# Performance work log

Hardware: AMD Instinct MI355X
Metric: run time of the kernel (lower is better)

Reference implementation:

```python
import jax, jax.numpy as jnp
import numpy as np

B = 8
NF = 64
COUNTS = [1200, 1400, 1500, 1536, 1600, 1700, 1800, 1552]  # ragged per-batch point counts
ND = 12288  # total decoder points (= sum(COUNTS))
NE = 12288  # total encoder points
LQ = 1800   # max per-batch count (padding length)
EPS = 1e-4  # scn BatchNormalization eps


def _build_geometry():
    """Random sparse 3D voxel coords per batch on a 64^3 grid; parent cells (coord//2)
    are unique by construction so the stride-2 downsample keeps one point per cell
    and Nkv == Nd with the same per-batch ordering (matches the module's slicing)."""
    rng = np.random.default_rng(0)
    coords = []
    for b, c in enumerate(COUNTS):
        cells = rng.choice(32 * 32 * 32, size=c, replace=False)
        x, y, z = cells // 1024, (cells // 32) % 32, cells % 32
        off = rng.integers(0, 2, size=(c, 3))
        pts = np.stack([x, y, z], 1) * 2 + off
        coords.append(np.concatenate([np.full((c, 1), b), pts], 1))
    coords = np.concatenate(coords, 0)  # [ND, 4] = (batch, x, y, z)
    lut = {tuple(r): i for i, r in enumerate(coords)}
    offs = np.array([[dx, dy, dz] for dx in (-1, 0, 1) for dy in (-1, 0, 1) for dz in (-1, 0, 1)])
    nbr = np.full((ND, 27), -1, np.int32)  # 3^3 submanifold rulebook
    for i, r in enumerate(coords):
        for k, o in enumerate(offs):
            j = lut.get((r[0], r[1] + o[0], r[2] + o[1], r[3] + o[2]))
            if j is not None:
                nbr[i, k] = j
    kv_nbr = np.full((ND, 8), -1, np.int32)  # stride-2 2^3 conv rulebook (1 child per cell)
    off_id = (coords[:, 1] % 2) * 4 + (coords[:, 2] % 2) * 2 + (coords[:, 3] % 2)
    kv_nbr[np.arange(ND), off_id] = np.arange(ND)
    pad_idx = np.full((B, LQ), -1, np.int32)
    unpad_idx = np.zeros(ND, np.int32)
    s = 0
    for b, c in enumerate(COUNTS):
        pad_idx[b, :c] = np.arange(s, s + c)
        unpad_idx[s:s + c] = b * LQ + np.arange(c)
        s += c
    return nbr, kv_nbr, pad_idx, unpad_idx


def setup_inputs() -> dict:
    nbr, kv_nbr, pad_idx, unpad_idx = _build_geometry()
    key = jax.random.key(0)
    ks = jax.random.split(key, 16)
    w = lambda k, i, o: jax.random.normal(k, (i, o), jnp.float32) / np.sqrt(i)
    w3 = lambda k, t, i, o: jax.random.normal(k, (t, i, o), jnp.float32) / np.sqrt(t * i)
    return {
        "x_decoder": jax.random.normal(ks[0], (ND, NF), jnp.float32),
        "x_encoder": jax.random.normal(ks[1], (NE, NF), jnp.float32),
        "Wp1": w(ks[2], NF, NF), "Wq": w(ks[3], NF, NF), "Wk": w(ks[4], NF, NF),
        "Wv": w(ks[5], NF, NF), "Wt": w(ks[6], NF, NF), "Wq1": w(ks[7], NF, NF),
        "Wk1": w(ks[8], NF, NF), "Wv1": w(ks[9], NF, NF),
        "Wdown": w3(ks[10], 8, NF, NF),
        "W3t": w3(ks[11], 27, NF, NF), "W3a": w3(ks[12], 27, NF, NF), "W3b": w3(ks[13], 27, NF, NF),
        "bn_gamma": jnp.ones((6, NF), jnp.float32),
        "bn_beta": jnp.zeros((6, NF), jnp.float32),
        "nbr": jnp.asarray(nbr), "kv_nbr": jnp.asarray(kv_nbr),
        "pad_idx": jnp.asarray(pad_idx), "unpad_idx": jnp.asarray(unpad_idx),
    }


def _bn(x, g, b):  # training-mode scn.BatchNormalization over all active points
    m = jnp.mean(x, 0)
    v = jnp.mean(jnp.square(x - m), 0)
    return (x - m) * jax.lax.rsqrt(v + EPS) * g + b


def _gconv(f, idx, W):  # rulebook sparse conv: idx [N,K] (-1 = missing), W [K,F,O]
    mask = (idx >= 0).astype(f.dtype)[..., None]
    g = f[jnp.clip(idx, 0)] * mask  # [N, K, F]
    return jnp.einsum('nkf,kfo->no', g, W)


def _pad(f, pad_idx):  # flat [N,F] -> padded [B,L,F] + validity mask [B,L]
    m = pad_idx >= 0
    return f[jnp.clip(pad_idx, 0)] * m[..., None].astype(f.dtype), m


def reference(x_decoder, x_encoder, Wp1, Wq, Wk, Wv, Wt, Wq1, Wk1, Wv1,
              Wdown, W3t, W3a, W3b, bn_gamma, bn_beta,
              nbr, kv_nbr, pad_idx, unpad_idx):
    xd = x_decoder @ Wp1                      # p1 (1x1 submanifold conv)
    q = xd @ Wq
    ke = x_encoder @ Wk
    ve = x_encoder @ Wv
    # Stage-1 cross attention. The torch loop slices queries per batch but always
    # uses the FULL encoder K/V (dk = features.T), so it equals one global attention.
    attn = jax.nn.softmax(q @ ke.T, axis=-1)  # [ND, NE], no 1/sqrt(d) scaling in source
    xr = (attn @ ve) @ Wt                     # trans_conv (1x1)
    xd = xd + _bn(xr, bn_gamma[0], bn_beta[0])  # after_norm residual add

    q1 = xd @ Wq1
    kv = _bn(_gconv(q1, kv_nbr, Wdown), bn_gamma[1], bn_beta[1])  # stride-2 conv + BN
    k1 = kv @ Wk1
    v1 = kv @ Wv1
    # Stage-2 ragged per-batch self attention (Nkv == Nd by construction).
    qp, _ = _pad(q1, pad_idx)                 # [B, LQ, NF]
    kp, mkv = _pad(k1, pad_idx)
    vp, _ = _pad(v1, pad_idx)
    s2 = jnp.einsum('blf,bmf->blm', qp, kp)
    s2 = jnp.where(mkv[:, None, :], s2, jnp.float32(-1e30))
    o = jnp.einsum('blm,bmf->blf', jax.nn.softmax(s2, axis=-1), vp)
    xr2 = o.reshape(B * LQ, NF)[unpad_idx]    # back to flat ragged layout [ND, NF]
    xr2 = _gconv(xr2, nbr, W3t)               # trans_conv1 (3^3 submanifold conv)
    xd = xd + _bn(xr2, bn_gamma[2], bn_beta[2])  # after_norm1 residual add

    # res block: BNReLU -> conv3 -> BNReLU -> conv3, add identity, BNReLU
    z = _gconv(jax.nn.relu(_bn(xd, bn_gamma[3], bn_beta[3])), nbr, W3a)
    z = _gconv(jax.nn.relu(_bn(z, bn_gamma[4], bn_beta[4])), nbr, W3b)
    return jax.nn.relu(_bn(xd + z, bn_gamma[5], bn_beta[5]))
```

## Files before the change

### kernel.cpp

```cpp
#include <hip/hip_runtime.h>

#define NPTS 12288
#define LQPAD 1800
#define LPAD2 1856
#define EPSBN 1e-4f
#define NSPLIT 8

typedef _Float16 half8 __attribute__((ext_vector_type(8)));
typedef _Float16 half4 __attribute__((ext_vector_type(4)));
typedef float floatx4 __attribute__((ext_vector_type(4)));

__global__ __launch_bounds__(256) void pack_all(const float* Wp1, const float* Wq, const float* Wk,
                                                const float* Wv, const float* Wt_, const float* Wq1,
                                                const float* Wk1, const float* Wv1, const float* Wdown,
                                                const float* W3t, const float* W3a, const float* W3b,
                                                const int* __restrict__ pad_idx, int* __restrict__ counts,
                                                _Float16* __restrict__ Wf) {
    int g = blockIdx.x;
    int t = threadIdx.x;
    if (g >= 97) {
        int b = g - 97;
        int s = 0;
        for (int i = t; i < LQPAD; i += 256) s += (pad_idx[b * LQPAD + i] >= 0) ? 1 : 0;
        for (int off = 32; off > 0; off >>= 1) s += __shfl_xor(s, off);
        if ((t & 63) == 0) atomicAdd(&counts[b], s);
        return;
    }
    int lane = t & 63, fg = t >> 6;
    int quad = lane >> 4, qi = lane & 15;
    if (g == 1) {
        __shared__ float A[4096], Bs[4096];
        for (int i = t; i < 4096; i += 256) {
            A[i] = Wp1[i];
            Bs[i] = Wq[i];
        }
        __syncthreads();
#pragma unroll
        for (int u = 0; u < 2; u++) {
            int frag = fg * 2 + u;
            int s = frag >> 2, ct = frag & 3;
            half8 v;
#pragma unroll
            for (int j = 0; j < 8; j++) {
                int r = s * 32 + quad * 8 + j, c = ct * 16 + qi;
                float acc = 0.f;
#pragma unroll
                for (int k = 0; k < 64; k++) acc += A[r * 64 + k] * Bs[k * 64 + c];
                v[j] = (_Float16)acc;
            }
            *(half8*)(Wf + (size_t)4096 + frag * 512 + lane * 8) = v;
        }
        return;
    }
    const float* src;
    if (g == 0) src = Wp1;
    else if (g == 2) src = Wk;
    else if (g == 3) src = Wv;
    else if (g == 4) src = Wt_;
    else if (g == 5) src = Wq1;
    else if (g == 6) src = Wk1;
    else if (g == 7) src = Wv1;
    else if (g < 16) src = Wdown + (size_t)(g - 8) * 4096;
    else if (g < 43) src = W3t + (size_t)(g - 16) * 4096;
    else if (g < 70) src = W3a + (size_t)(g - 43) * 4096;
    else src = W3b + (size_t)(g - 70) * 4096;
#pragma unroll
    for (int u = 0; u < 2; u++) {
        int frag = fg * 2 + u;
        int s = frag >> 2, ct = frag & 3;
        half8 v;
#pragma unroll
        for (int j = 0; j < 8; j++) v[j] = (_Float16)src[(s * 32 + quad * 8 + j) * 64 + ct * 16 + qi];
        *(half8*)(Wf + (size_t)g * 4096 + frag * 512 + lane * 8) = v;
    }
}

__device__ inline void load_split8(const float* p, half8& hi, half8& lo) {
    float4 a = *(const float4*)p;
    float4 b = *(const float4*)(p + 4);
    float v[8] = {a.x, a.y, a.z, a.w, b.x, b.y, b.z, b.w};
#pragma unroll
    for (int j = 0; j < 8; j++) {
        _Float16 h = (_Float16)v[j];
        hi[j] = h;
        lo[j] = (_Float16)(v[j] - (float)h);
    }
}

__global__ __launch_bounds__(256) void gemm_head(const float* __restrict__ xdec, const float* __restrict__ xenc,
                                                 const _Float16* __restrict__ Wf, float* __restrict__ xd,
                                                 _Float16* __restrict__ Qh,
                                                 _Float16* __restrict__ Kh, _Float16* __restrict__ Vt) {
    int z = blockIdx.y;
    const float* A = (z < 2) ? xdec : xenc;
    const _Float16* Bf = Wf + (size_t)z * 4096;
    int t = threadIdx.x;
    int lane = t & 63, wv = t >> 6;
    int quad = lane >> 4, qi = lane & 15;
    int row0w = blockIdx.x * 64 + wv * 16;
    half8 ah[2], al[2];
#pragma unroll
    for (int s = 0; s < 2; s++) load_split8(A + (size_t)(row0w + qi) * 64 + s * 32 + quad * 8, ah[s], al[s]);
    floatx4 C[4];
#pragma unroll
    for (int ct = 0; ct < 4; ct++) C[ct] = floatx4{0.f, 0.f, 0.f, 0.f};
#pragma unroll
    for (int ct = 0; ct < 4; ct++)
#pragma unroll
        for (int s = 0; s < 2; s++) {
            half8 b = *(const half8*)(Bf + (s * 4 + ct) * 512 + lane * 8);
            C[ct] = __builtin_amdgcn_mfma_f32_16x16x32_f16(ah[s], b, C[ct], 0, 0, 0);
            C[ct] = __builtin_amdgcn_mfma_f32_16x16x32_f16(al[s], b, C[ct], 0, 0, 0);
        }
    int orow = row0w + quad * 4;
    if (z == 0) {
#pragma unroll
        for (int ct = 0; ct < 4; ct++)
#pragma unroll
            for (int r = 0; r < 4; r++) xd[(size_t)(orow + r) * 64 + ct * 16 + qi] = C[ct][r];
    } else if (z == 1) {
#pragma unroll
        for (int ct = 0; ct < 4; ct++)
#pragma unroll
            for (int r = 0; r < 4; r++) Qh[(size_t)(orow + r) * 64 + ct * 16 + qi] = (_Float16)C[ct][r];
    } else if (z == 2) {
#pragma unroll
        for (int ct = 0; ct < 4; ct++)
#pragma unroll
            for (int r = 0; r < 4; r++) Kh[(size_t)(orow + r) * 64 + ct * 16 + qi] = (_Float16)C[ct][r];
    } else {
#pragma unroll
        for (int ct = 0; ct < 4; ct++) {
            half4 o;
#pragma unroll
            for (int r = 0; r < 4; r++) o[r] = (_Float16)C[ct][r];
            *(half4*)(Vt + (size_t)(ct * 16 + qi) * NPTS + orow) = o;
        }
    }
}

__global__ __launch_bounds__(256) void gemm_q1(const float* __restrict__ xr, float* __restrict__ xd,
                                               const _Float16* __restrict__ Bf,
                                               const float* __restrict__ stats,
                                               const float* __restrict__ gamma,
                                               const float* __restrict__ beta,
                                               _Float16* __restrict__ Oh) {
    int t = threadIdx.x;
    int lane = t & 63, wv = t >> 6;
    int quad = lane >> 4, qi = lane & 15;
    int row0w = blockIdx.x * 64 + wv * 16;
    const float inv_n = 1.f / (float)NPTS;
    half8 ah[2], al[2];
#pragma unroll
    for (int s = 0; s < 2; s++) {
        size_t base = (size_t)(row0w + qi) * 64 + s * 32 + quad * 8;
        float4 xa = *(const float4*)(xr + base);
        float4 xb = *(const float4*)(xr + base + 4);
        float4 da = *(const float4*)(xd + base);
        float4 db = *(const float4*)(xd + base + 4);
        float vx[8] = {xa.x, xa.y, xa.z, xa.w, xb.x, xb.y, xb.z, xb.w};
        float vd[8] = {da.x, da.y, da.z, da.w, db.x, db.y, db.z, db.w};
        float vo[8];
#pragma unroll
        for (int j = 0; j < 8; j++) {
            int f = s * 32 + quad * 8 + j;
            float mean = stats[f] * inv_n;
            float var = stats[64 + f] * inv_n - mean * mean;
            float val = vd[j] + (vx[j] - mean) * rsqrtf(var + EPSBN) * gamma[f] + beta[f];
            vo[j] = val;
            _Float16 h = (_Float16)val;
            ah[s][j] = h;
            al[s][j] = (_Float16)(val - (float)h);
        }
        *(float4*)(xd + base) = float4{vo[0], vo[1], vo[2], vo[3]};
        *(float4*)(xd + base + 4) = float4{vo[4], vo[5], vo[6], vo[7]};
    }
    floatx4 C[4];
#pragma unroll
    for (int ct = 0; ct < 4; ct++) C[ct] = floatx4{0.f, 0.f, 0.f, 0.f};
#pragma unroll
    for (int ct = 0; ct < 4; ct++)
#pragma unroll
        for (int s = 0; s < 2; s++) {
            half8 b = *(const half8*)(Bf + (s * 4 + ct) * 512 + lane * 8);
            C[ct] = __builtin_amdgcn_mfma_f32_16x16x32_f16(ah[s], b, C[ct], 0, 0, 0);
            C[ct] = __builtin_amdgcn_mfma_f32_16x16x32_f16(al[s], b, C[ct], 0, 0, 0);
        }
    int orow = row0w + quad * 4;
#pragma unroll
    for (int ct = 0; ct < 4; ct++)
#pragma unroll
        for (int r = 0; r < 4; r++) Oh[(size_t)(orow + r) * 64 + ct * 16 + qi] = (_Float16)C[ct][r];
}

__global__ __launch_bounds__(256) void gemm_kv1(const float* __restrict__ kv, const _Float16* __restrict__ Wfk,
                                                const _Float16* __restrict__ Wfv,
                                                const float* __restrict__ stats, const float* __restrict__ gamma,
                                                const float* __restrict__ beta, const int* __restrict__ unpad,
                                                _Float16* __restrict__ Kh1, _Float16* __restrict__ Vt2) {
    int y = blockIdx.y;
    int t = threadIdx.x;
    int lane = t & 63, wv = t >> 6;
    int quad = lane >> 4, qi = lane & 15;
    int row0w = blockIdx.x * 64 + wv * 16;
    const float inv_n = 1.f / (float)NPTS;
    half8 ah[2], al[2];
#pragma unroll
    for (int s = 0; s < 2; s++) {
        const float* p = kv + (size_t)(row0w + qi) * 64 + s * 32 + quad * 8;
        float4 a = *(const float4*)p;
        float4 b2 = *(const float4*)(p + 4);
        float v[8] = {a.x, a.y, a.z, a.w, b2.x, b2.y, b2.z, b2.w};
#pragma unroll
        for (int j = 0; j < 8; j++) {
            int f = s * 32 + quad * 8 + j;
            float mean = stats[f] * inv_n;
            float var = stats[64 + f] * inv_n - mean * mean;
            float val = (v[j] - mean) * rsqrtf(var + EPSBN) * gamma[f] + beta[f];
            _Float16 h = (_Float16)val;
            ah[s][j] = h;
            al[s][j] = (_Float16)(val - (float)h);
        }
    }
    const _Float16* Bf = y ? Wfv : Wfk;
    floatx4 C[4];
#pragma unroll
    for (int ct = 0; ct < 4; ct++) C[ct] = floatx4{0.f, 0.f, 0.f, 0.f};
#pragma unroll
    for (int ct = 0; ct < 4; ct++)
#pragma unroll
        for (int s = 0; s < 2; s++) {
            half8 b = *(const half8*)(Bf + (s * 4 + ct) * 512 + lane * 8);
            C[ct] = __builtin_amdgcn_mfma_f32_16x16x32_f16(ah[s], b, C[ct], 0, 0, 0);
            C[ct] = __builtin_amdgcn_mfma_f32_16x16x32_f16(al[s], b, C[ct], 0, 0, 0);
        }
    int orow = row0w + quad * 4;
    if (y == 0) {
#pragma unroll
        for (int ct = 0; ct < 4; ct++)
#pragma unroll
            for (int r = 0; r < 4; r++) Kh1[(size_t)(orow + r) * 64 + ct * 16 + qi] = (_Float16)C[ct][r];
    } else {
        int u0 = unpad[orow], u3 = unpad[orow + 3];
        int b0 = u0 / 1800, b3 = u3 / 1800;
        if (u3 == u0 + 3 && b0 == b3) {
            int p0 = u0 - b0 * 1800;
#pragma unroll
            for (int ct = 0; ct < 4; ct++) {
                half4 o;
#pragma unroll
                for (int r = 0; r < 4; r++) o[r] = (_Float16)C[ct][r];
                *(half4*)(Vt2 + ((size_t)b0 * 64 + ct * 16 + qi) * LPAD2 + p0) = o;
            }
        } else {
#pragma unroll
            for (int r = 0; r < 4; r++) {
                int u = unpad[orow + r];
                int b = u / 1800, p = u - b * 1800;
#pragma unroll
                for (int ct = 0; ct < 4; ct++)
                    Vt2[((size_t)b * 64 + ct * 16 + qi) * LPAD2 + p] = (_Float16)C[ct][r];
            }
        }
    }
}

__global__ __launch_bounds__(256) void gconv_mfma(const _Float16* __restrict__ Xh,
                                                  const int* __restrict__ idx,
                                                  const _Float16* __restrict__ Wf,
                                                  float* __restrict__ OUT, int nk,
                                                  const float* Xadd, float* stats_out) {
    __shared__ float s_sum[64], s_ss[64];
    int t = threadIdx.x;
    int lane = t & 63, wv = t >> 6;
    int quad = lane >> 4, qi = lane & 15;
    int bx = blockIdx.x;
    int row0 = (bx >> 1) * 64 + wv * 16;
    int cb = (bx & 1) * 2;
    if (stats_out) {
        if (t < 64) {
            s_sum[t] = 0.f;
            s_ss[t] = 0.f;
        }
        __syncthreads();
    }
    floatx4 Oacc[2];
#pragma unroll
    for (int u = 0; u < 2; u++) Oacc[u] = floatx4{0.f, 0.f, 0.f, 0.f};
    const int* ip = idx + (size_t)(row0 + qi) * nk;
    int j = ip[0];
    half8 a0 = half8{0, 0, 0, 0, 0, 0, 0, 0};
    half8 a1 = half8{0, 0, 0, 0, 0, 0, 0, 0};
    if (j >= 0) {
        a0 = *(const half8*)(Xh + (size_t)j * 64 + quad * 8);
        a1 = *(const half8*)(Xh + (size_t)j * 64 + 32 + quad * 8);
    }
    for (int k = 0; k < nk; k++) {
        half8 n0 = half8{0, 0, 0, 0, 0, 0, 0, 0};
        half8 n1 = half8{0, 0, 0, 0, 0, 0, 0, 0};
        if (k + 1 < nk) {
            int jn = ip[k + 1];
            if (jn >= 0) {
                n0 = *(const half8*)(Xh + (size_t)jn * 64 + quad * 8);
                n1 = *(const half8*)(Xh + (size_t)jn * 64 + 32 + quad * 8);
            }
        }
        const _Float16* wk = Wf + (size_t)k * 4096;
#pragma unroll
        for (int u = 0; u < 2; u++) {
            int ct = cb + u;
            half8 b0 = *(const half8*)(wk + ct * 512 + lane * 8);
            half8 b1 = *(const half8*)(wk + (4 + ct) * 512 + lane * 8);
            Oacc[u] = __builtin_amdgcn_mfma_f32_16x16x32_f16(a0, b0, Oacc[u], 0, 0, 0);
            Oacc[u] = __builtin_amdgcn_mfma_f32_16x16x32_f16(a1, b1, Oacc[u], 0, 0, 0);
        }
        a0 = n0;
        a1 = n1;
    }
    int orow = row0 + quad * 4;
#pragma unroll
    for (int u = 0; u < 2; u++) {
        int ct = cb + u;
#pragma unroll
        for (int r = 0; r < 4; r++) OUT[(size_t)(orow + r) * 64 + ct * 16 + qi] = Oacc[u][r];
    }
    if (stats_out) {
#pragma unroll
        for (int u = 0; u < 2; u++) {
            int f = (cb + u) * 16 + qi;
            float ps = 0.f, pss = 0.f;
#pragma unroll
            for (int r = 0; r < 4; r++) {
                float v = Oacc[u][r];
                if (Xadd) v += Xadd[(size_t)(orow + r) * 64 + f];
                ps += v;
                pss += v * v;
            }
            atomicAdd(&s_sum[f], ps);
            atomicAdd(&s_ss[f], pss);
        }
        __syncthreads();
        if (t < 64) {
            atomicAdd(&stats_out[t], s_sum[t]);
            atomicAdd(&stats_out[64 + t], s_ss[t]);
        }
    }
}

__global__ __launch_bounds__(256) void bn_apply(const float* __restrict__ X, const float* X2,
                                                const float* R, float* OUT, _Float16* OUT16,
                                                const float* __restrict__ stats,
                                                const float* __restrict__ gamma,
                                                const float* __restrict__ beta,
                                                float* stats_out, int n, int do_relu) {
    __shared__ float sh[2][4][64];
    int t = threadIdx.x;
    int f = t & 63, g = t >> 6;
    float inv_n = 1.f / (float)n;
    float mean = stats[f] * inv_n;
    float var = stats[64 + f] * inv_n - mean * mean;
    float rstd = rsqrtf(var + EPSBN);
    float ga = gamma[f], be = beta[f];
    float s = 0.f, ss = 0.f;
    for (int r = blockIdx.x * 4 + g; r < n; r += gridDim.x * 4) {
        size_t i = (size_t)r * 64 + f;
        float v = X[i];
        if (X2) v += X2[i];
        v = (v - mean) * rstd * ga + be;
        if (R) v += R[i];
        if (do_relu) v = fmaxf(v, 0.f);
        if (OUT) OUT[i] = v;
        if (OUT16) OUT16[i] = (_Float16)v;
        s += v;
        ss += v * v;
    }
    if (stats_out) {
        sh[0][g][f] = s;
        sh[1][g][f] = ss;
        __syncthreads();
        if (g == 0) {
            s = sh[0][0][f] + sh[0][1][f] + sh[0][2][f] + sh[0][3][f];
            ss = sh[1][0][f] + sh[1][1][f] + sh[1][2][f] + sh[1][3][f];
            atomicAdd(&stats_out[f], s);
            atomicAdd(&stats_out[64 + f], ss);
        }
    }
}

__global__ __launch_bounds__(256, 3) void flash1_mfma(const _Float16* __restrict__ Qh,
                                                      const _Float16* __restrict__ Kh,
                                                      const _Float16* __restrict__ Vt,
                                                      _Float16* __restrict__ Op,
                                                      float* __restrict__ Ms,
                                                      float* __restrict__ Ls) {
    __shared__ __align__(16) _Float16 KsF[8 * 512];
    __shared__ __align__(16) _Float16 VsF[8 * 512];
    __shared__ __align__(16) _Float16 PTF[4][2 * 1024];
    int t = threadIdx.x;
    int lane = t & 63, wv = t >> 6;
    int quad = lane >> 4, qi = lane & 15;
    int qb = blockIdx.x, sp = blockIdx.y;
    int q0w = qb * 128 + wv * 32;

    half8 qh[2][2];
#pragma unroll
    for (int sub = 0; sub < 2; sub++)
#pragma unroll
        for (int s = 0; s < 2; s++) {
            int qrow = q0w + sub * 16 + qi;
            qh[sub][s] = *(const half8*)(Qh + (size_t)qrow * 64 + s * 32 + quad * 8);
        }
    floatx4 Oacc[2][4];
#pragma unroll
    for (int sub = 0; sub < 2; sub++)
#pragma unroll
        for (int ft = 0; ft < 4; ft++) Oacc[sub][ft] = floatx4{0.f, 0.f, 0.f, 0.f};
    float m_i[2] = {-1e30f, -1e30f}, l_i[2] = {0.f, 0.f};

    for (int it = 0; it < 24; it++) {
        int k0 = sp * 1536 + it * 64;
        __syncthreads();
#pragma unroll
        for (int u = 0; u < 4; u++) {
            int frag = wv + 4 * u;
            if (frag < 8) {
                int kt = frag >> 1, s = frag & 1;
                int key = k0 + kt * 16 + qi;
                *(half8*)(KsF + frag * 512 + lane * 8) =
                    *(const half8*)(Kh + (size_t)key * 64 + s * 32 + quad * 8);
            } else {
                int fr = frag - 8;
                int ft = fr >> 1, s = fr & 1;
                int f = ft * 16 + qi;
                *(half8*)(VsF + fr * 512 + lane * 8) =
                    *(const half8*)(Vt + (size_t)f * NPTS + k0 + s * 32 + quad * 8);
            }
        }
        __syncthreads();
        half8 ka[4][2];
#pragma unroll
        for (int kt = 0; kt < 4; kt++)
#pragma unroll
            for (int s = 0; s < 2; s++) ka[kt][s] = *(const half8*)(KsF + (kt * 2 + s) * 512 + lane * 8);
        floatx4 st[2][4];
#pragma unroll
        for (int sub = 0; sub < 2; sub++)
#pragma unroll
            for (int kt = 0; kt < 4; kt++) {
                floatx4 acc = floatx4{0.f, 0.f, 0.f, 0.f};
#pragma unroll
                for (int s = 0; s < 2; s++)
                    acc = __builtin_amdgcn_mfma_f32_16x16x32_f16(ka[kt][s], qh[sub][s], acc, 0, 0, 0);
                st[sub][kt] = acc;
            }
#pragma unroll
        for (int sub = 0; sub < 2; sub++) {
            float mloc = -1e30f;
#pragma unroll
            for (int kt = 0; kt < 4; kt++)
#pragma unroll
                for (int r = 0; r < 4; r++) mloc = fmaxf(mloc, st[sub][kt][r]);
            mloc = fmaxf(mloc, __shfl_xor(mloc, 16));
            mloc = fmaxf(mloc, __shfl_xor(mloc, 32));
            float m_new = fmaxf(m_i[sub], mloc);
            float ps = 0.f;
#pragma unroll
            for (int kt = 0; kt < 4; kt++) {
                half4 pk;
#pragma unroll
                for (int r = 0; r < 4; r++) {
                    float p = __expf(st[sub][kt][r] - m_new);
                    ps += p;
                    pk[r] = (_Float16)p;
                }
                int s = kt >> 1;
                int qd2 = (kt & 1) * 2 + (quad >> 1);
                *(half4*)(&PTF[wv][sub * 1024 + (s * 64 + qd2 * 16 + qi) * 8 + (quad & 1) * 4]) = pk;
            }
            ps += __shfl_xor(ps, 16);
            ps += __shfl_xor(ps, 32);
            if (m_new > m_i[sub]) {
                float alpha = __expf(m_i[sub] - m_new);
                l_i[sub] = l_i[sub] * alpha + ps;
                m_i[sub] = m_new;
#pragma unroll
                for (int ft = 0; ft < 4; ft++) Oacc[sub][ft] *= alpha;
            } else {
                l_i[sub] += ps;
            }
        }
        half8 pb[2][2];
#pragma unroll
        for (int sub = 0; sub < 2; sub++)
#pragma unroll
            for (int s = 0; s < 2; s++)
                pb[sub][s] = *(const half8*)(&PTF[wv][sub * 1024 + (s * 64 + lane) * 8]);
#pragma unroll
        for (int ft = 0; ft < 4; ft++)
#pragma unroll
            for (int s = 0; s < 2; s++) {
                half8 v = *(const half8*)(VsF + (ft * 2 + s) * 512 + lane * 8);
                Oacc[0][ft] = __builtin_amdgcn_mfma_f32_16x16x32_f16(v, pb[0][s], Oacc[0][ft], 0, 0, 0);
                Oacc[1][ft] = __builtin_amdgcn_mfma_f32_16x16x32_f16(v, pb[1][s], Oacc[1][ft], 0, 0, 0);
            }
    }
#pragma unroll
    for (int sub = 0; sub < 2; sub++) {
#pragma unroll
        for (int ft = 0; ft < 4; ft++) {
            half4 o;
#pragma unroll
            for (int r = 0; r < 4; r++) o[r] = (_Float16)Oacc[sub][ft][r];
            *(half4*)(Op + ((size_t)sp * NPTS + q0w + sub * 16 + qi) * 64 + ft * 16 + quad * 4) = o;
        }
        if (lane < 16) {
            Ms[sp * NPTS + q0w + sub * 16 + lane] = m_i[sub];
            Ls[sp * NPTS + q0w + sub * 16 + lane] = l_i[sub];
        }
    }
}

__global__ __launch_bounds__(256) void merge_gemm(const _Float16* __restrict__ Op,
                                                  const float* __restrict__ Ms, const float* __restrict__ Ls,
                                                  const _Float16* __restrict__ Wtf,
                                                  float* __restrict__ xr, float* __restrict__ stats_out) {
    __shared__ float w12[64][NSPLIT];
    __shared__ float Linv[64];
    __shared__ __align__(16) _Float16 Ah[64 * 72], Al[64 * 72];
    __shared__ float s_sum[64], s_ss[64];
    int t = threadIdx.x;
    int row0 = blockIdx.x * 64;
    if (t < 64) {
        int q = row0 + t;
        float m[NSPLIT], M = -1e30f;
#pragma unroll
        for (int s = 0; s < NSPLIT; s++) {
            m[s] = Ms[s * NPTS + q];
            M = fmaxf(M, m[s]);
        }
        float L = 0.f;
#pragma unroll
        for (int s = 0; s < NSPLIT; s++) {
            float w = __expf(m[s] - M);
            w12[t][s] = w;
            L += Ls[s * NPTS + q] * w;
        }
        Linv[t] = 1.f / L;
        s_sum[t] = 0.f;
        s_ss[t] = 0.f;
    }
    __syncthreads();
    for (int k = 0; k < 4; k++) {
        int i = t + k * 256;
        int qr = i >> 4, f4 = (i & 15) * 4;
        int q = row0 + qr;
        float acc[4] = {0.f, 0.f, 0.f, 0.f};
#pragma unroll
        for (int s = 0; s < NSPLIT; s++) {
            float w = w12[qr][s];
            half4 o = *(const half4*)(Op + ((size_t)s * NPTS + q) * 64 + f4);
#pragma unroll
            for (int c = 0; c < 4; c++) acc[c] += (float)o[c] * w;
        }
        float inv = Linv[qr];
#pragma unroll
        for (int c = 0; c < 4; c++) {
            float val = acc[c] * inv;
            _Float16 h = (_Float16)val;
            Ah[qr * 72 + f4 + c] = h;
            Al[qr * 72 + f4 + c] = (_Float16)(val - (float)h);
        }
    }
    __syncthreads();
    int lane = t & 63, wv = t >> 6;
    int quad = lane >> 4, qi = lane & 15;
    int rloc = wv * 16 + qi;
    half8 ah[2], al[2];
#pragma unroll
    for (int s = 0; s < 2; s++) {
        ah[s] = *(const half8*)(Ah + rloc * 72 + s * 32 + quad * 8);
        al[s] = *(const half8*)(Al + rloc * 72 + s * 32 + quad * 8);
    }
    floatx4 C[4];
#pragma unroll
    for (int ct = 0; ct < 4; ct++) C[ct] = floatx4{0.f, 0.f, 0.f, 0.f};
#pragma unroll
    for (int ct = 0; ct < 4; ct++)
#pragma unroll
        for (int s = 0; s < 2; s++) {
            half8 b = *(const half8*)(Wtf + (s * 4 + ct) * 512 + lane * 8);
            C[ct] = __builtin_amdgcn_mfma_f32_16x16x32_f16(ah[s], b, C[ct], 0, 0, 0);
            C[ct] = __builtin_amdgcn_mfma_f32_16x16x32_f16(al[s], b, C[ct], 0, 0, 0);
        }
    int orow = row0 + wv * 16 + quad * 4;
#pragma unroll
    for (int ct = 0; ct < 4; ct++) {
        int f = ct * 16 + qi;
        float ps = 0.f, pss = 0.f;
#pragma unroll
        for (int r = 0; r < 4; r++) {
            float v = C[ct][r];
            xr[(size_t)(orow + r) * 64 + f] = v;
            ps += v;
            pss += v * v;
        }
        atomicAdd(&s_sum[f], ps);
        atomicAdd(&s_ss[f], pss);
    }
    __syncthreads();
    if (t < 64) {
        atomicAdd(&stats_out[t], s_sum[t]);
        atomicAdd(&stats_out[64 + t], s_ss[t]);
    }
}

__global__ __launch_bounds__(256) void flash2_mfma(const _Float16* __restrict__ Qh,
                                                   const _Float16* __restrict__ Kh,
                                                   const _Float16* __restrict__ Vt2,
                                                   const int* __restrict__ pad_idx,
                                                   const int* __restrict__ counts,
                                                   _Float16* __restrict__ O) {
    int b = blockIdx.y;
    int c = counts[b];
    int qb = blockIdx.x;
    if (qb * 64 >= c) return;
    __shared__ __align__(16) _Float16 KsF[8 * 512];
    __shared__ __align__(16) _Float16 VsF[8 * 512];
    __shared__ __align__(16) _Float16 PTF[4][2 * 512];
    int t = threadIdx.x;
    int lane = t & 63, wv = t >> 6;
    int quad = lane >> 4, qi = lane & 15;
    const int* prow = pad_idx + b * LQPAD;
    int p_q = qb * 64 + wv * 16 + qi;
    int flat_q = (p_q < LQPAD) ? prow[p_q] : -1;

    half8 qh[2];
#pragma unroll
    for (int s = 0; s < 2; s++) {
        qh[s] = (flat_q >= 0) ? *(const half8*)(Qh + (size_t)flat_q * 64 + s * 32 + quad * 8)
                              : half8{0, 0, 0, 0, 0, 0, 0, 0};
    }
    floatx4 Oacc[4];
#pragma unroll
    for (int ft = 0; ft < 4; ft++) Oacc[ft] = floatx4{0.f, 0.f, 0.f, 0.f};
    float m_i = -1e30f, l_i = 0.f;
    const _Float16* VtB = Vt2 + (size_t)b * 64 * LPAD2;

    int nt = (c + 63) >> 6;
    for (int it = 0; it < nt; it++) {
        int k0 = it * 64;
        __syncthreads();
#pragma unroll
        for (int u = 0; u < 4; u++) {
            int frag = wv + 4 * u;
            if (frag < 8) {
                int kt = frag >> 1, s = frag & 1;
                int kp = k0 + kt * 16 + qi;
                int flat = (kp < c) ? prow[kp] : -1;
                int d0 = s * 32 + quad * 8;
                half8 kvv = half8{0, 0, 0, 0, 0, 0, 0, 0};
                if (flat >= 0) kvv = *(const half8*)(Kh + (size_t)flat * 64 + d0);
                *(half8*)(KsF + frag * 512 + lane * 8) = kvv;
            } else {
                int fr = frag - 8;
                int ft = fr >> 1, s = fr & 1;
                int f = ft * 16 + qi;
                int key = k0 + s * 32 + quad * 8;
                *(half8*)(VsF + fr * 512 + lane * 8) = *(const half8*)(VtB + f * LPAD2 + key);
            }
        }
        __syncthreads();
        floatx4 st[4];
#pragma unroll
        for (int kt = 0; kt < 4; kt++) {
            floatx4 acc = floatx4{0.f, 0.f, 0.f, 0.f};
#pragma unroll
            for (int s = 0; s < 2; s++) {
                half8 a = *(const half8*)(KsF + (kt * 2 + s) * 512 + lane * 8);
                acc = __builtin_amdgcn_mfma_f32_16x16x32_f16(a, qh[s], acc, 0, 0, 0);
            }
            st[kt] = acc;
        }
        float mloc = -1e30f;
#pragma unroll
        for (int kt = 0; kt < 4; kt++)
#pragma unroll
            for (int r = 0; r < 4; r++) mloc = fmaxf(mloc, st[kt][r]);
        mloc = fmaxf(mloc, __shfl_xor(mloc, 16));
        mloc = fmaxf(mloc, __shfl_xor(mloc, 32));
        float m_new = fmaxf(m_i, mloc);
        float ps = 0.f;
#pragma unroll
        for (int kt = 0; kt < 4; kt++) {
            half4 pk;
#pragma unroll
            for (int r = 0; r < 4; r++) {
                int kpos = k0 + kt * 16 + quad * 4 + r;
                float p = (kpos < c) ? __expf(st[kt][r] - m_new) : 0.f;
                ps += p;
                pk[r] = (_Float16)p;
            }
            int s = kt >> 1;
            int qd2 = (kt & 1) * 2 + (quad >> 1);
            *(half4*)(&PTF[wv][(s * 64 + qd2 * 16 + qi) * 8 + (quad & 1) * 4]) = pk;
        }
        ps += __shfl_xor(ps, 16);
        ps += __shfl_xor(ps, 32);
        if (m_new > m_i) {
            float alpha = __expf(m_i - m_new);
            l_i = l_i * alpha + ps;
            m_i = m_new;
#pragma unroll
            for (int ft = 0; ft < 4; ft++) Oacc[ft] *= alpha;
        } else {
            l_i += ps;
        }
        half8 pb[2];
#pragma unroll
        for (int s = 0; s < 2; s++) pb[s] = *(const half8*)(&PTF[wv][(s * 64 + lane) * 8]);
#pragma unroll
        for (int ft = 0; ft < 4; ft++)
#pragma unroll
            for (int s = 0; s < 2; s++) {
                half8 a = *(const half8*)(VsF + (ft * 2 + s) * 512 + lane * 8);
                Oacc[ft] = __builtin_amdgcn_mfma_f32_16x16x32_f16(a, pb[s], Oacc[ft], 0, 0, 0);
            }
    }
    if (flat_q >= 0) {
        float inv = 1.f / l_i;
#pragma unroll
        for (int ft = 0; ft < 4; ft++) {
            half4 o;
#pragma unroll
            for (int r = 0; r < 4; r++) o[r] = (_Float16)(Oacc[ft][r] * inv);
            *(half4*)(O + (size_t)flat_q * 64 + ft * 16 + quad * 4) = o;
        }
    }
}

extern "C" void kernel_launch(void* const* d_in, const int* in_sizes, int n_in,
                              void* d_out, int out_size, void* d_ws, size_t ws_size,
                              hipStream_t stream) {
    const float* x_dec = (const float*)d_in[0];
    const float* x_enc = (const float*)d_in[1];
    const float* Wp1 = (const float*)d_in[2];
    const float* Wq = (const float*)d_in[3];
    const float* Wk = (const float*)d_in[4];
    const float* Wv = (const float*)d_in[5];
    const float* Wt_ = (const float*)d_in[6];
    const float* Wq1 = (const float*)d_in[7];
    const float* Wk1 = (const float*)d_in[8];
    const float* Wv1 = (const float*)d_in[9];
    const float* Wdown = (const float*)d_in[10];
    const float* W3t = (const float*)d_in[11];
    const float* W3a = (const float*)d_in[12];
    const float* W3b = (const float*)d_in[13];
    const float* bn_g = (const float*)d_in[14];
    const float* bn_b = (const float*)d_in[15];
    const int* nbr = (const int*)d_in[16];
    const int* kv_nbr = (const int*)d_in[17];
    const int* pad_idx = (const int*)d_in[18];
    const int* unpad_idx = (const int*)d_in[19];
    float* out = (float*)d_out;
    float* ws = (float*)d_ws;

    const int N = NPTS;
    const size_t BUF = (size_t)N * 64;
    float* xd = ws;
    float* s1 = ws + 1 * BUF;
    float* s2 = ws + 2 * BUF;
    float* s3 = ws + 3 * BUF;
    float* s4 = ws + 4 * BUF;
    float* s5 = ws + 5 * BUF;
    float* s6 = ws + 6 * BUF;
    float* s7 = ws + 7 * BUF;
    float* s8 = ws + 8 * BUF;
    float* arena = ws + 9 * BUF;

    float* stats = arena;
    int* counts = (int*)(arena + 768);
    float* Ms = arena + 1024;
    float* Ls = Ms + (size_t)NSPLIT * NPTS;
    _Float16* WfA = (_Float16*)(Ls + (size_t)NSPLIT * NPTS);

    _Float16* Oph = (_Float16*)s1;
    _Float16* Qh = (_Float16*)s7;
    _Float16* Kh = (_Float16*)s8;
    _Float16* Vt = Kh + BUF;
    float* xr = s8;
    _Float16* Qh1 = (_Float16*)s7;
    float* kv = s1;
    _Float16* Kh1 = (_Float16*)s2;
    _Float16* Vt2 = (_Float16*)s3;
    _Float16* z2h = (_Float16*)s4;
    float* xr2 = s5;
    _Float16* xrh = (_Float16*)s6;
    float* o2 = s1;
    _Float16* xr2h = (_Float16*)s2;
    float* z2 = s3;

    const _Float16* Wtf = WfA + 4 * 4096;
    const _Float16* Wq1f = WfA + 5 * 4096;
    const _Float16* Wk1f = WfA + 6 * 4096;
    const _Float16* Wv1f = WfA + 7 * 4096;
    const _Float16* Wdf = WfA + 8 * 4096;
    const _Float16* W3tf = WfA + (size_t)16 * 4096;
    const _Float16* W3af = WfA + (size_t)43 * 4096;
    const _Float16* W3bf = WfA + (size_t)70 * 4096;

    hipMemsetAsync(stats, 0, 1024 * sizeof(float), stream);

    dim3 B(256);
    int gG = N / 64;
    int gC2 = 2 * gG;

    pack_all<<<105, B, 0, stream>>>(Wp1, Wq, Wk, Wv, Wt_, Wq1, Wk1, Wv1, Wdown, W3t, W3a, W3b,
                                    pad_idx, counts, WfA);

    gemm_head<<<dim3(gG, 4), B, 0, stream>>>(x_dec, x_enc, WfA, xd, Qh, Kh, Vt);
    flash1_mfma<<<dim3(N / 128, NSPLIT), B, 0, stream>>>(Qh, Kh, Vt, Oph, Ms, Ls);
    merge_gemm<<<gG, B, 0, stream>>>(Oph, Ms, Ls, Wtf, xr, stats + 0);
    gemm_q1<<<gG, B, 0, stream>>>(xr, xd, Wq1f, stats + 0, bn_g + 0, bn_b + 0, Qh1);

    gconv_mfma<<<gC2, B, 0, stream>>>(Qh1, kv_nbr, Wdf, kv, 8, nullptr, stats + 128);
    gemm_kv1<<<dim3(gG, 2), B, 0, stream>>>(kv, Wk1f, Wv1f, stats + 128, bn_g + 64, bn_b + 64,
                                            unpad_idx, Kh1, Vt2);
    flash2_mfma<<<dim3(LPAD2 / 64, 8), B, 0, stream>>>(Qh1, Kh1, Vt2, pad_idx, counts, z2h);
    gconv_mfma<<<gC2, B, 0, stream>>>(z2h, nbr, W3tf, xr2, 27, nullptr, stats + 256);
    bn_apply<<<256, B, 0, stream>>>(xr2, nullptr, xd, xd, nullptr, stats + 256, bn_g + 128, bn_b + 128,
                                    stats + 384, N, 0);

    bn_apply<<<256, B, 0, stream>>>(xd, nullptr, nullptr, nullptr, xrh, stats + 384, bn_g + 192,
                                    bn_b + 192, nullptr, N, 1);
    gconv_mfma<<<gC2, B, 0, stream>>>(xrh, nbr, W3af, o2, 27, nullptr, stats + 512);
    bn_apply<<<256, B, 0, stream>>>(o2, nullptr, nullptr, nullptr, xr2h, stats + 512, bn_g + 256,
                                    bn_b + 256, nullptr, N, 1);
    gconv_mfma<<<gC2, B, 0, stream>>>(xr2h, nbr, W3bf, z2, 27, xd, stats + 640);
    bn_apply<<<256, B, 0, stream>>>(xd, z2, nullptr, out, nullptr, stats + 640, bn_g + 320, bn_b + 320,
                                    nullptr, N, 1);
}
```

Baseline: 409.3 us.

## Fuse BN+ReLU into gather conv and use exp2 with pre-scaled queries

```diff
diff --git a/kernel.cpp b/kernel.cpp
--- a/kernel.cpp
+++ b/kernel.cpp
@@ -5,6 +5,13 @@
 #define LPAD2 1856
 #define EPSBN 1e-4f
 #define NSPLIT 8
+#define LOG2E 1.44269504088896340736f
+
+#if __has_builtin(__builtin_amdgcn_exp2f)
+#define EXP2F __builtin_amdgcn_exp2f
+#else
+#define EXP2F exp2f
+#endif
 
 typedef _Float16 half8 __attribute__((ext_vector_type(8)));
 typedef _Float16 half4 __attribute__((ext_vector_type(4)));
@@ -122,7 +129,8 @@
 #pragma unroll
         for (int ct = 0; ct < 4; ct++)
 #pragma unroll
-            for (int r = 0; r < 4; r++) Qh[(size_t)(orow + r) * 64 + ct * 16 + qi] = (_Float16)C[ct][r];
+            for (int r = 0; r < 4; r++)
+                Qh[(size_t)(orow + r) * 64 + ct * 16 + qi] = (_Float16)(C[ct][r] * LOG2E);
     } else if (z == 2) {
 #pragma unroll
         for (int ct = 0; ct < 4; ct++)
@@ -344,6 +352,130 @@
             atomicAdd(&stats_out[t], s_sum[t]);
             atomicAdd(&stats_out[64 + t], s_ss[t]);
         }
+    }
+}
+
+__global__ __launch_bounds__(256) void gconv_bn_mfma(const float* __restrict__ X,
+                                                     const int* __restrict__ idx,
+                                                     const _Float16* __restrict__ Wf,
+                                                     float* __restrict__ OUT, int nk,
+                                                     const float* __restrict__ stats,
+                                                     const float* __restrict__ gamma,
+                                                     const float* __restrict__ beta,
+                                                     const float* Xadd, float* stats_out) {
+    __shared__ float s_sum[64], s_ss[64];
+    int t = threadIdx.x;
+    int lane = t & 63, wv = t >> 6;
+    int quad = lane >> 4, qi = lane & 15;
+    int bx = blockIdx.x;
+    int row0 = (bx >> 1) * 64 + wv * 16;
+    int cb = (bx & 1) * 2;
+    if (t < 64) {
+        s_sum[t] = 0.f;
+        s_ss[t] = 0.f;
+    }
+    __syncthreads();
+    const float inv_n = 1.f / (float)NPTS;
+    float sc[2][8], sh[2][8];
+#pragma unroll
+    for (int s = 0; s < 2; s++)
+#pragma unroll
+        for (int jj = 0; jj < 8; jj++) {
+            int f = s * 32 + quad * 8 + jj;
+            float mean = stats[f] * inv_n;
+            float var = stats[64 + f] * inv_n - mean * mean;
+            float rs = rsqrtf(var + EPSBN) * gamma[f];
+            sc[s][jj] = rs;
+            sh[s][jj] = beta[f] - mean * rs;
+        }
+    floatx4 Oacc[2];
+#pragma unroll
+    for (int u = 0; u < 2; u++) Oacc[u] = floatx4{0.f, 0.f, 0.f, 0.f};
+    const int* ip = idx + (size_t)(row0 + qi) * nk;
+    float cur[16];
+    int jvalid;
+    {
+        int j0 = ip[0];
+        jvalid = (j0 >= 0);
+        if (jvalid) {
+            const float* p = X + (size_t)j0 * 64 + quad * 8;
+            float4 x0 = *(const float4*)p;
+            float4 x1 = *(const float4*)(p + 4);
+            float4 x2 = *(const float4*)(p + 32);
+            float4 x3 = *(const float4*)(p + 36);
+            cur[0] = x0.x; cur[1] = x0.y; cur[2] = x0.z; cur[3] = x0.w;
+            cur[4] = x1.x; cur[5] = x1.y; cur[6] = x1.z; cur[7] = x1.w;
+            cur[8] = x2.x; cur[9] = x2.y; cur[10] = x2.z; cur[11] = x2.w;
+            cur[12] = x3.x; cur[13] = x3.y; cur[14] = x3.z; cur[15] = x3.w;
+        }
+    }
+    for (int k = 0; k < nk; k++) {
+        half8 a0, a1;
+        if (jvalid) {
+#pragma unroll
+            for (int e = 0; e < 8; e++) {
+                a0[e] = (_Float16)fmaxf(cur[e] * sc[0][e] + sh[0][e], 0.f);
+                a1[e] = (_Float16)fmaxf(cur[8 + e] * sc[1][e] + sh[1][e], 0.f);
+            }
+        } else {
+            a0 = half8{0, 0, 0, 0, 0, 0, 0, 0};
+            a1 = half8{0, 0, 0, 0, 0, 0, 0, 0};
+        }
+        int nvalid = 0;
+        float nxt[16];
+        if (k + 1 < nk) {
+            int jn = ip[k + 1];
+            nvalid = (jn >= 0);
+            if (nvalid) {
+                const float* p = X + (size_t)jn * 64 + quad * 8;
+                float4 x0 = *(const float4*)p;
+                float4 x1 = *(const float4*)(p + 4);
+                float4 x2 = *(const float4*)(p + 32);
+                float4 x3 = *(const float4*)(p + 36);
+                nxt[0] = x0.x; nxt[1] = x0.y; nxt[2] = x0.z; nxt[3] = x0.w;
+                nxt[4] = x1.x; nxt[5] = x1.y; nxt[6] = x1.z; nxt[7] = x1.w;
+                nxt[8] = x2.x; nxt[9] = x2.y; nxt[10] = x2.z; nxt[11] = x2.w;
+                nxt[12] = x3.x; nxt[13] = x3.y; nxt[14] = x3.z; nxt[15] = x3.w;
+            }
+        }
+        const _Float16* wk = Wf + (size_t)k * 4096;
+#pragma unroll
+        for (int u = 0; u < 2; u++) {
+            int ct = cb + u;
+            half8 b0 = *(const half8*)(wk + ct * 512 + lane * 8);
+            half8 b1 = *(const half8*)(wk + (4 + ct) * 512 + lane * 8);
+            Oacc[u] = __builtin_amdgcn_mfma_f32_16x16x32_f16(a0, b0, Oacc[u], 0, 0, 0);
+            Oacc[u] = __builtin_amdgcn_mfma_f32_16x16x32_f16(a1, b1, Oacc[u], 0, 0, 0);
+        }
+        jvalid = nvalid;
+#pragma unroll
+        for (int e = 0; e < 16; e++) cur[e] = nxt[e];
+    }
+    int orow = row0 + quad * 4;
+#pragma unroll
+    for (int u = 0; u < 2; u++) {
+        int ct = cb + u;
+#pragma unroll
+        for (int r = 0; r < 4; r++) OUT[(size_t)(orow + r) * 64 + ct * 16 + qi] = Oacc[u][r];
+    }
+#pragma unroll
+    for (int u = 0; u < 2; u++) {
+        int f = (cb + u) * 16 + qi;
+        float ps = 0.f, pss = 0.f;
+#pragma unroll
+        for (int r = 0; r < 4; r++) {
+            float v = Oacc[u][r];
+            if (Xadd) v += Xadd[(size_t)(orow + r) * 64 + f];
+            ps += v;
+            pss += v * v;
+        }
+        atomicAdd(&s_sum[f], ps);
+        atomicAdd(&s_ss[f], pss);
+    }
+    __syncthreads();
+    if (t < 64) {
+        atomicAdd(&stats_out[t], s_sum[t]);
+        atomicAdd(&stats_out[64 + t], s_ss[t]);
     }
 }
 
@@ -469,7 +601,7 @@
                 half4 pk;
 #pragma unroll
                 for (int r = 0; r < 4; r++) {
-                    float p = __expf(st[sub][kt][r] - m_new);
+                    float p = EXP2F(st[sub][kt][r] - m_new);
                     ps += p;
                     pk[r] = (_Float16)p;
                 }
@@ -480,7 +612,7 @@
             ps += __shfl_xor(ps, 16);
             ps += __shfl_xor(ps, 32);
             if (m_new > m_i[sub]) {
-                float alpha = __expf(m_i[sub] - m_new);
+                float alpha = EXP2F(m_i[sub] - m_new);
                 l_i[sub] = l_i[sub] * alpha + ps;
                 m_i[sub] = m_new;
 #pragma unroll
@@ -541,7 +673,7 @@
         float L = 0.f;
 #pragma unroll
         for (int s = 0; s < NSPLIT; s++) {
-            float w = __expf(m[s] - M);
+            float w = EXP2F(m[s] - M);
             w12[t][s] = w;
             L += Ls[s * NPTS + q] * w;
         }
@@ -772,7 +904,6 @@
     float* s3 = ws + 3 * BUF;
     float* s4 = ws + 4 * BUF;
     float* s5 = ws + 5 * BUF;
-    float* s6 = ws + 6 * BUF;
     float* s7 = ws + 7 * BUF;
     float* s8 = ws + 8 * BUF;
     float* arena = ws + 9 * BUF;
@@ -794,9 +925,7 @@
     _Float16* Vt2 = (_Float16*)s3;
     _Float16* z2h = (_Float16*)s4;
     float* xr2 = s5;
-    _Float16* xrh = (_Float16*)s6;
     float* o2 = s1;
-    _Float16* xr2h = (_Float16*)s2;
     float* z2 = s3;
 
     const _Float16* Wtf = WfA + 4 * 4096;
@@ -830,12 +959,10 @@
     bn_apply<<<256, B, 0, stream>>>(xr2, nullptr, xd, xd, nullptr, stats + 256, bn_g + 128, bn_b + 128,
                                     stats + 384, N, 0);
 
-    bn_apply<<<256, B, 0, stream>>>(xd, nullptr, nullptr, nullptr, xrh, stats + 384, bn_g + 192,
-                                    bn_b + 192, nullptr, N, 1);
-    gconv_mfma<<<gC2, B, 0, stream>>>(xrh, nbr, W3af, o2, 27, nullptr, stats + 512);
-    bn_apply<<<256, B, 0, stream>>>(o2, nullptr, nullptr, nullptr, xr2h, stats + 512, bn_g + 256,
-                                    bn_b + 256, nullptr, N, 1);
-    gconv_mfma<<<gC2, B, 0, stream>>>(xr2h, nbr, W3bf, z2, 27, xd, stats + 640);
+    gconv_bn_mfma<<<gC2, B, 0, stream>>>(xd, nbr, W3af, o2, 27, stats + 384, bn_g + 192, bn_b + 192,
+                                         nullptr, stats + 512);
+    gconv_bn_mfma<<<gC2, B, 0, stream>>>(o2, nbr, W3bf, z2, 27, stats + 512, bn_g + 256, bn_b + 256,
+                                         xd, stats + 640);
     bn_apply<<<256, B, 0, stream>>>(xd, z2, nullptr, out, nullptr, stats + 640, bn_g + 320, bn_b + 320,
                                     nullptr, N, 1);
 }
```

Result: faster. 398.5 us (median of 2 runs) (-2.6%).
